# Optimization experiments

Hardware: AMD Instinct MI355X
Metric: run time of the kernel (lower is better)

## Reference

```python
import jax, jax.numpy as jnp
import numpy as np

D_IN = 1024
D_OUT = 1024
NUM_HEADS = 16
HEAD_DIM = D_OUT // NUM_HEADS


def setup_inputs() -> dict:
    key = jax.random.key(0)
    ks = jax.random.split(key, 6)
    s = 0.02
    x = jax.random.normal(ks[0], (1, 4096, D_IN), dtype=jnp.float32)
    W_q = jax.random.normal(ks[1], (D_IN, D_OUT), dtype=jnp.float32) * s
    W_k = jax.random.normal(ks[2], (D_IN, D_OUT), dtype=jnp.float32) * s
    W_v = jax.random.normal(ks[3], (D_IN, D_OUT), dtype=jnp.float32) * s
    W_o = jax.random.normal(ks[4], (D_OUT, D_OUT), dtype=jnp.float32) * s
    b_o = jnp.zeros((D_OUT,), dtype=jnp.float32)
    return {"x": x, "W_q": W_q, "W_k": W_k, "W_v": W_v, "W_o": W_o, "b_o": b_o}


def reference(x, W_q, W_k, W_v, W_o, b_o):
    b, n, _ = x.shape
    # project and split heads: [b, h, n, d]
    def split_heads(t):
        return t.reshape(b, n, NUM_HEADS, HEAD_DIM).transpose(0, 2, 1, 3)
    q = split_heads(x @ W_q)
    k = split_heads(x @ W_k)
    v = split_heads(x @ W_v)
    scale = 1.0 / jnp.sqrt(jnp.float32(HEAD_DIM))
    scores = jnp.einsum('bhqd,bhkd->bhqk', q, k) * scale  # [b,h,n,n]
    causal = jnp.tril(jnp.ones((n, n), dtype=bool))
    scores = jnp.where(causal, scores, -jnp.inf)
    weights = jax.nn.softmax(scores, axis=-1)
    # dropout rate is 0.0 -> identity
    ctx = jnp.einsum('bhqk,bhkd->bhqd', weights, v)
    ctx = ctx.transpose(0, 2, 1, 3).reshape(b, n, D_OUT)
    return ctx @ W_o + b_o
```

## Files before the change

### kernel.cpp

```cpp
#include <hip/hip_runtime.h>
#include <hip/hip_bf16.h>

typedef __hip_bfloat16 bf16;
typedef __attribute__((ext_vector_type(8))) short short8;
typedef __attribute__((ext_vector_type(4))) float floatx4;

#define SEQ 4096
#define DIM 1024
#define NH 16
#define HD 64

#if defined(__has_builtin)
#if __has_builtin(__builtin_amdgcn_exp2f)
#define EXP2(x) __builtin_amdgcn_exp2f(x)
#endif
#endif
#ifndef EXP2
#define EXP2(x) exp2f(x)
#endif

__device__ __forceinline__ short f2s(float f) { bf16 t = __float2bfloat16(f); return *(short*)&t; }

__device__ __forceinline__ void gload16(const void* g, void* l) {
    __builtin_amdgcn_global_load_lds(
        (const __attribute__((address_space(1))) void*)g,
        (__attribute__((address_space(3))) void*)l, 16, 0, 0);
}

__device__ __forceinline__ void barrier_lgkm() {
    asm volatile("s_waitcnt lgkmcnt(0)" ::: "memory");
    __builtin_amdgcn_s_barrier();
}

__device__ __forceinline__ short8 cvt8(float4 a, float4 b) {
    short8 s;
    s[0] = f2s(a.x); s[1] = f2s(a.y); s[2] = f2s(a.z); s[3] = f2s(a.w);
    s[4] = f2s(b.x); s[5] = f2s(b.y); s[6] = f2s(b.z); s[7] = f2s(b.w);
    return s;
}

__global__ __launch_bounds__(256) void transpose_cast_kernel(
    const float* __restrict__ W0, const float* __restrict__ W1,
    const float* __restrict__ W2, const float* __restrict__ W3,
    bf16* __restrict__ Wt_all)
{
    const float* W = blockIdx.z == 0 ? W0 : blockIdx.z == 1 ? W1
                   : blockIdx.z == 2 ? W2 : W3;
    bf16* Wt = Wt_all + (size_t)blockIdx.z * DIM * DIM;

    __shared__ float tile[32][33];
    const int n0 = blockIdx.x * 32, k0 = blockIdx.y * 32;
    const int tr = threadIdx.x >> 5;
    const int tc = threadIdx.x & 31;
#pragma unroll
    for (int i = 0; i < 32; i += 8)
        tile[tr + i][tc] = W[(size_t)(k0 + tr + i) * DIM + n0 + tc];
    __syncthreads();
#pragma unroll
    for (int i = 0; i < 32; i += 8)
        Wt[(size_t)(n0 + tr + i) * DIM + k0 + tc] = __float2bfloat16(tile[tc][tr + i]);
}

#define QBM 128
#define QBN 128
#define QBK 64

__global__ __launch_bounds__(256) void qkv_gemm_kernel(
    const float* __restrict__ A, const bf16* __restrict__ Wt,
    bf16* __restrict__ Qb, bf16* __restrict__ Kb, bf16* __restrict__ Vb)
{
    const int z = blockIdx.z;
    const bf16* Bt = Wt + (size_t)z * DIM * DIM;
    bf16* C = z == 0 ? Qb : (z == 1 ? Kb : Vb);
    const float osc = (z == 0) ? 0.18033688f : 1.0f;

    __shared__ alignas(16) float Af[QBM][QBK];
    __shared__ alignas(16) short Bs[QBN][QBK];

    const int tid  = threadIdx.x;
    const int wave = tid >> 6, lane = tid & 63;
    const int l15  = lane & 15, quad = lane >> 4;
    const int wm = (wave & 1) * 64;
    const int wn = (wave >> 1) * 64;
    const int bm = blockIdx.y * QBM;
    const int bn = blockIdx.x * QBN;

    const int arow = tid >> 4;
    const int agch = (tid & 15) ^ (arow & 15);
    const float* gA = A + (size_t)(bm + arow) * DIM + agch * 4;
    char* ldsA = (char*)&Af[0][0] + wave * 1024;

    const int brow = tid >> 3;
    const int bgch = (tid & 7) ^ (brow & 7);
    const bf16* gB = Bt + (size_t)(bn + brow) * DIM + bgch * 8;
    char* ldsB = (char*)&Bs[0][0] + wave * 1024;

    floatx4 acc[4][4] = {};

    for (int k0 = 0; k0 < DIM; k0 += QBK) {
        __syncthreads();
#pragma unroll
        for (int c = 0; c < 8; ++c)
            gload16(gA + (size_t)c * 16 * DIM + k0, ldsA + c * 4096);
#pragma unroll
        for (int c = 0; c < 4; ++c)
            gload16(gB + (size_t)c * 32 * DIM + k0, ldsB + c * 4096);
        __syncthreads();

#pragma unroll
        for (int c2 = 0; c2 < 2; ++c2) {
            const int g0 = c2 * 8 + quad * 2;
            const int cb = (c2 * 4 + quad) ^ (l15 & 7);
            short8 afr[4], bfr[4];
#pragma unroll
            for (int i = 0; i < 4; ++i) {
                const int ra = wm + i * 16 + l15;
                float4 f0 = *(const float4*)&Af[ra][(g0 ^ l15) * 4];
                float4 f1 = *(const float4*)&Af[ra][((g0 + 1) ^ l15) * 4];
                afr[i] = cvt8(f0, f1);
                bfr[i] = *(const short8*)&Bs[wn + i * 16 + l15][cb * 8];
            }
#pragma unroll
            for (int mi = 0; mi < 4; ++mi)
#pragma unroll
                for (int ni = 0; ni < 4; ++ni)
                    acc[mi][ni] = __builtin_amdgcn_mfma_f32_16x16x32_bf16(
                        afr[mi], bfr[ni], acc[mi][ni], 0, 0, 0);
        }
    }

#pragma unroll
    for (int mi = 0; mi < 4; ++mi)
#pragma unroll
        for (int r = 0; r < 4; ++r) {
            const int row = bm + wm + mi * 16 + quad * 4 + r;
#pragma unroll
            for (int ni = 0; ni < 4; ++ni) {
                const int col = bn + wn + ni * 16 + l15;
                C[(size_t)row * DIM + col] = __float2bfloat16(acc[mi][ni][r] * osc);
            }
        }
}

__global__ __launch_bounds__(256) void out_gemm_kernel(
    const bf16* __restrict__ A, const bf16* __restrict__ Bt,
    const float* __restrict__ bias, float* __restrict__ C)
{
    __shared__ alignas(16) short Asl[128][64];
    __shared__ alignas(16) short Bsl[64][64];

    const int tid  = threadIdx.x;
    const int wave = tid >> 6, lane = tid & 63;
    const int l15  = lane & 15, quad = lane >> 4;
    const int wm = (wave & 1) * 64;
    const int wn = (wave >> 1) * 32;
    const int bm = blockIdx.y * 128;
    const int bn = blockIdx.x * 64;

    const int srow   = tid >> 3;
    const int gchunk = (tid & 7) ^ (srow & 7);
    const bf16* gA = A  + (size_t)(bm + srow) * DIM + gchunk * 8;
    const bf16* gB = Bt + (size_t)(bn + srow) * DIM + gchunk * 8;
    char* ldsA = (char*)&Asl[0][0] + wave * 1024;
    char* ldsB = (char*)&Bsl[0][0] + wave * 1024;

    floatx4 acc[4][2] = {};

    for (int k0 = 0; k0 < DIM; k0 += 64) {
        __syncthreads();
#pragma unroll
        for (int c = 0; c < 4; ++c)
            gload16(gA + (size_t)c * 32 * DIM + k0, ldsA + c * 4096);
#pragma unroll
        for (int c = 0; c < 2; ++c)
            gload16(gB + (size_t)c * 32 * DIM + k0, ldsB + c * 4096);
        __syncthreads();

#pragma unroll
        for (int c2 = 0; c2 < 2; ++c2) {
            const int cb = (c2 * 4 + quad) ^ (l15 & 7);
            short8 afr[4], bfr[2];
#pragma unroll
            for (int i = 0; i < 4; ++i)
                afr[i] = *(const short8*)&Asl[wm + i * 16 + l15][cb * 8];
#pragma unroll
            for (int i = 0; i < 2; ++i)
                bfr[i] = *(const short8*)&Bsl[wn + i * 16 + l15][cb * 8];
#pragma unroll
            for (int mi = 0; mi < 4; ++mi)
#pragma unroll
                for (int ni = 0; ni < 2; ++ni)
                    acc[mi][ni] = __builtin_amdgcn_mfma_f32_16x16x32_bf16(
                        afr[mi], bfr[ni], acc[mi][ni], 0, 0, 0);
        }
    }

#pragma unroll
    for (int mi = 0; mi < 4; ++mi)
#pragma unroll
        for (int r = 0; r < 4; ++r) {
            const int row = bm + wm + mi * 16 + quad * 4 + r;
#pragma unroll
            for (int ni = 0; ni < 2; ++ni) {
                const int col = bn + wn + ni * 16 + l15;
                C[(size_t)row * DIM + col] = acc[mi][ni][r] + bias[col];
            }
        }
}

#define QT 128
#define KT 64
#define LDT 72

__global__ __launch_bounds__(512, 4) void flash_attn_kernel(
    const bf16* __restrict__ Q, const bf16* __restrict__ K,
    const bf16* __restrict__ V, bf16* ctx)
{
    const int lin  = blockIdx.y * 32 + blockIdx.x;
    const int half = lin >> 8, idx = lin & 255;
    const int qj   = half ? (idx & 31) : 31 - (idx & 31);
    const int h    = (idx >> 5) + 8 * half;
    const int q0   = qj * QT;
    const int nkt  = 2 * qj + 2;

    const int tid  = threadIdx.x;
    const int wave = tid >> 6;
    const int qg   = wave & 3;
    const int kh   = wave >> 2;
    const int lane = tid & 63;
    const int l15  = lane & 15;
    const int quad = lane >> 4;

    __shared__ alignas(16) char smem[36864];
    short (*Ks)[KT][LDT] = (short (*)[KT][LDT])smem;
    short (*Vt)[HD][LDT] = (short (*)[HD][LDT])(smem + 18432);
    float* redO = (float*)smem;
    float* redL = (float*)(smem + 32768);

    short8 qfrag[2][2];
#pragma unroll
    for (int s = 0; s < 2; ++s) {
        const bf16* qp = Q + (size_t)(q0 + qg * 32 + s * 16 + l15) * DIM
                       + h * HD + quad * 8;
        qfrag[s][0] = *(const short8*)(qp);
        qfrag[s][1] = *(const short8*)(qp + 32);
    }

    const int kr = tid >> 3, kc = (tid & 7) * 8;
    const bool vstager = tid < 256;
    const int vr = (tid & 31) * 2, vd = ((tid >> 5) & 7) * 8;
    const int vcol = (vr & 32) + ((vr >> 2) & 3) * 8
                   + ((vr >> 4) & 1) * 4 + (vr & 3);

    short8 kreg, vreg0, vreg1;
    kreg = *(const short8*)(K + (size_t)kr * DIM + h * HD + kc);
    if (vstager) {
        vreg0 = *(const short8*)(V + (size_t)vr * DIM + h * HD + vd);
        vreg1 = *(const short8*)(V + (size_t)(vr + 1) * DIM + h * HD + vd);
    }
    *(short8*)&Ks[0][kr][kc] = kreg;
    if (vstager) {
#pragma unroll
        for (int i = 0; i < 8; ++i) {
            unsigned int pv = (unsigned int)(unsigned short)vreg0[i]
                            | ((unsigned int)(unsigned short)vreg1[i] << 16);
            *(unsigned int*)&Vt[0][vd + i][vcol] = pv;
        }
    }
    kreg = *(const short8*)(K + (size_t)(KT + kr) * DIM + h * HD + kc);
    if (vstager) {
        vreg0 = *(const short8*)(V + (size_t)(KT + vr) * DIM + h * HD + vd);
        vreg1 = *(const short8*)(V + (size_t)(KT + vr + 1) * DIM + h * HD + vd);
    }

    barrier_lgkm();

    short8 onesf;
#pragma unroll
    for (int i = 0; i < 8; ++i) onesf[i] = (short)0x3F80;

    floatx4 o_acc[2][4] = {};
    floatx4 lacc[2] = {};

    for (int kt = 0; kt < nkt; ++kt) {
        const int b = kt & 1;

        floatx4 sT[2][2] = {};
#pragma unroll
        for (int n = 0; n < 2; ++n)
#pragma unroll
            for (int c = 0; c < 2; ++c) {
                short8 kf = *(const short8*)
                    &Ks[b][kh * 32 + n * 16 + l15][c * 32 + quad * 8];
#pragma unroll
                for (int s = 0; s < 2; ++s)
                    sT[s][n] = __builtin_amdgcn_mfma_f32_16x16x32_bf16(
                        kf, qfrag[s][c], sT[s][n], 0, 0, 0);
            }

        if (kt + 1 < nkt) {
            *(short8*)&Ks[b ^ 1][kr][kc] = kreg;
            if (vstager) {
#pragma unroll
                for (int i = 0; i < 8; ++i) {
                    unsigned int pv = (unsigned int)(unsigned short)vreg0[i]
                                    | ((unsigned int)(unsigned short)vreg1[i] << 16);
                    *(unsigned int*)&Vt[b ^ 1][vd + i][vcol] = pv;
                }
            }
            if (kt + 2 < nkt) {
                const size_t nb = (size_t)(kt + 2) * KT;
                kreg = *(const short8*)(K + (nb + kr) * DIM + h * HD + kc);
                if (vstager) {
                    vreg0 = *(const short8*)(V + (nb + vr) * DIM + h * HD + vd);
                    vreg1 = *(const short8*)(V + (nb + vr + 1) * DIM + h * HD + vd);
                }
            }
        }

        short8 pfrag[2];
        const int kbase = kt * KT + kh * 32;
        if (kt >= nkt - 2) {
#pragma unroll
            for (int s = 0; s < 2; ++s) {
                const int qrow = q0 + qg * 32 + s * 16 + l15;
                float p[2][4];
#pragma unroll
                for (int n = 0; n < 2; ++n) {
                    const int key0 = kbase + n * 16 + quad * 4;
#pragma unroll
                    for (int r = 0; r < 4; ++r)
                        p[n][r] = (key0 + r <= qrow) ? EXP2(sT[s][n][r]) : 0.f;
                }
                short8 f;
#pragma unroll
                for (int j = 0; j < 8; ++j)
                    f[j] = f2s(p[j >> 2][j & 3]);
                pfrag[s] = f;
            }
        } else {
#pragma unroll
            for (int s = 0; s < 2; ++s) {
                short8 f;
#pragma unroll
                for (int j = 0; j < 8; ++j)
                    f[j] = f2s(EXP2(sT[s][j >> 2][j & 3]));
                pfrag[s] = f;
            }
        }

#pragma unroll
        for (int n = 0; n < 4; ++n) {
            short8 vf = *(const short8*)
                &Vt[b][n * 16 + l15][kh * 32 + quad * 8];
#pragma unroll
            for (int s = 0; s < 2; ++s)
                o_acc[s][n] = __builtin_amdgcn_mfma_f32_16x16x32_bf16(
                    pfrag[s], vf, o_acc[s][n], 0, 0, 0);
        }
#pragma unroll
        for (int s = 0; s < 2; ++s)
            lacc[s] = __builtin_amdgcn_mfma_f32_16x16x32_bf16(
                pfrag[s], onesf, lacc[s], 0, 0, 0);

        barrier_lgkm();
    }

    if (kh == 1) {
#pragma unroll
        for (int s = 0; s < 2; ++s)
#pragma unroll
            for (int n = 0; n < 4; ++n)
#pragma unroll
                for (int r = 0; r < 4; ++r)
                    redO[(size_t)(qg * 32 + s * 16 + quad * 4 + r) * 64
                         + n * 16 + l15] = o_acc[s][n][r];
        if (l15 == 0) {
#pragma unroll
            for (int s = 0; s < 2; ++s)
#pragma unroll
                for (int r = 0; r < 4; ++r)
                    redL[qg * 32 + s * 16 + quad * 4 + r] = lacc[s][r];
        }
    }
    __syncthreads();
    if (kh == 0) {
#pragma unroll
        for (int s = 0; s < 2; ++s)
#pragma unroll
            for (int r = 0; r < 4; ++r) {
                const int row_l = qg * 32 + s * 16 + quad * 4 + r;
                const float lsum = lacc[s][r] + redL[row_l];
                const float inv = 1.0f / lsum;
                const int row = q0 + row_l;
#pragma unroll
                for (int n = 0; n < 4; ++n) {
                    const float o = o_acc[s][n][r]
                                  + redO[(size_t)row_l * 64 + n * 16 + l15];
                    ctx[(size_t)row * DIM + h * HD + n * 16 + l15] =
                        __float2bfloat16(o * inv);
                }
            }
    }
}

extern "C" void kernel_launch(void* const* d_in, const int* in_sizes, int n_in,
                              void* d_out, int out_size, void* d_ws, size_t ws_size,
                              hipStream_t stream)
{
    const float* x  = (const float*)d_in[0];
    const float* Wq = (const float*)d_in[1];
    const float* Wk = (const float*)d_in[2];
    const float* Wv = (const float*)d_in[3];
    const float* Wo = (const float*)d_in[4];
    const float* bo = (const float*)d_in[5];
    float* out = (float*)d_out;

    bf16* Wt_all = (bf16*)d_ws;
    bf16* Qb     = Wt_all + (size_t)4 * DIM * DIM;
    bf16* V      = (bf16*)d_out;
    bf16* Kb     = V + (size_t)SEQ * DIM;
    bf16* ctx    = Qb;
    const bf16* Wot = Wt_all + (size_t)3 * DIM * DIM;

    transpose_cast_kernel<<<dim3(32, 32, 4), 256, 0, stream>>>(Wq, Wk, Wv, Wo, Wt_all);

    qkv_gemm_kernel<<<dim3(DIM / QBN, SEQ / QBM, 3), 256, 0, stream>>>(
        x, Wt_all, Qb, Kb, V);

    flash_attn_kernel<<<dim3(32, NH), 512, 0, stream>>>(Qb, Kb, V, ctx);

    out_gemm_kernel<<<dim3(DIM / 64, SEQ / 128), 256, 0, stream>>>(
        ctx, Wot, bo, out);
}
```

Baseline: 184.3 us.

## Software-pipeline flash attention: overlap QK^T of next tile with PV of previous

Restructures the attention loop into a two-stage software pipeline: each iteration computes S for tile p while finishing exp/PV for tile p-1, using a triple-buffered LDS ring for K and V^T. The aim is to hide the exp/convert latency behind independent MFMA work and to keep the matrix units busy. In exchange it raises LDS use from 36KB to 54KB per block, which may lower occupancy under launch_bounds(512,4), and adds live registers for the carried score tile.

```diff
diff --git a/kernel.cpp b/kernel.cpp
--- a/kernel.cpp
+++ b/kernel.cpp
@@ -211,6 +211,7 @@
 #define QT 128
 #define KT 64
 #define LDT 72
+#define BUFB 18432
 
 __global__ __launch_bounds__(512, 4) void flash_attn_kernel(
     const bf16* __restrict__ Q, const bf16* __restrict__ K,
@@ -231,9 +232,9 @@
     const int l15  = lane & 15;
     const int quad = lane >> 4;
 
-    __shared__ alignas(16) char smem[36864];
-    short (*Ks)[KT][LDT] = (short (*)[KT][LDT])smem;
-    short (*Vt)[HD][LDT] = (short (*)[HD][LDT])(smem + 18432);
+    __shared__ alignas(16) char smem[3 * BUFB];
+#define KSB(b) ((short(*)[LDT])(smem + (size_t)(b) * BUFB))
+#define VTB(b) ((short(*)[LDT])(smem + (size_t)(b) * BUFB + 9216))
     float* redO = (float*)smem;
     float* redL = (float*)(smem + 32768);
 
@@ -258,13 +259,13 @@
         vreg0 = *(const short8*)(V + (size_t)vr * DIM + h * HD + vd);
         vreg1 = *(const short8*)(V + (size_t)(vr + 1) * DIM + h * HD + vd);
     }
-    *(short8*)&Ks[0][kr][kc] = kreg;
+    *(short8*)&KSB(0)[kr][kc] = kreg;
     if (vstager) {
 #pragma unroll
         for (int i = 0; i < 8; ++i) {
             unsigned int pv = (unsigned int)(unsigned short)vreg0[i]
                             | ((unsigned int)(unsigned short)vreg1[i] << 16);
-            *(unsigned int*)&Vt[0][vd + i][vcol] = pv;
+            *(unsigned int*)&VTB(0)[vd + i][vcol] = pv;
         }
     }
     kreg = *(const short8*)(K + (size_t)(KT + kr) * DIM + h * HD + kc);
@@ -281,35 +282,93 @@
 
     floatx4 o_acc[2][4] = {};
     floatx4 lacc[2] = {};
-
-    for (int kt = 0; kt < nkt; ++kt) {
-        const int b = kt & 1;
-
-        floatx4 sT[2][2] = {};
+    floatx4 sTp[2][2] = {};
+
+#define FINISH(t) do {                                                        \
+    short(*_Vtb)[LDT] = VTB((t) % 3);                                         \
+    short8 _vf[4];                                                            \
+    _Pragma("unroll")                                                         \
+    for (int _n = 0; _n < 4; ++_n)                                            \
+        _vf[_n] = *(const short8*)&_Vtb[_n * 16 + l15][kh * 32 + quad * 8];   \
+    short8 _pf[2];                                                            \
+    const int _kbase = (t) * KT + kh * 32;                                    \
+    if ((t) >= nkt - 2) {                                                     \
+        _Pragma("unroll")                                                     \
+        for (int _s = 0; _s < 2; ++_s) {                                      \
+            const int _qrow = q0 + qg * 32 + _s * 16 + l15;                   \
+            float _p[2][4];                                                   \
+            _Pragma("unroll")                                                 \
+            for (int _n = 0; _n < 2; ++_n) {                                  \
+                const int _k0 = _kbase + _n * 16 + quad * 4;                  \
+                _Pragma("unroll")                                             \
+                for (int _r = 0; _r < 4; ++_r)                                \
+                    _p[_n][_r] = (_k0 + _r <= _qrow)                          \
+                               ? EXP2(sTp[_s][_n][_r]) : 0.f;                 \
+            }                                                                 \
+            short8 _f;                                                        \
+            _Pragma("unroll")                                                 \
+            for (int _j = 0; _j < 8; ++_j)                                    \
+                _f[_j] = f2s(_p[_j >> 2][_j & 3]);                            \
+            _pf[_s] = _f;                                                     \
+        }                                                                     \
+    } else {                                                                  \
+        _Pragma("unroll")                                                     \
+        for (int _s = 0; _s < 2; ++_s) {                                      \
+            short8 _f;                                                        \
+            _Pragma("unroll")                                                 \
+            for (int _j = 0; _j < 8; ++_j)                                    \
+                _f[_j] = f2s(EXP2(sTp[_s][_j >> 2][_j & 3]));                 \
+            _pf[_s] = _f;                                                     \
+        }                                                                     \
+    }                                                                         \
+    _Pragma("unroll")                                                         \
+    for (int _n = 0; _n < 4; ++_n)                                            \
+        _Pragma("unroll")                                                     \
+        for (int _s = 0; _s < 2; ++_s)                                        \
+            o_acc[_s][_n] = __builtin_amdgcn_mfma_f32_16x16x32_bf16(          \
+                _pf[_s], _vf[_n], o_acc[_s][_n], 0, 0, 0);                    \
+    _Pragma("unroll")                                                         \
+    for (int _s = 0; _s < 2; ++_s)                                            \
+        lacc[_s] = __builtin_amdgcn_mfma_f32_16x16x32_bf16(                   \
+            _pf[_s], onesf, lacc[_s], 0, 0, 0);                               \
+} while (0)
+
+    for (int p = 0; p < nkt; ++p) {
+        short(*Ksb)[LDT] = KSB(p % 3);
+
+        short8 kf[2][2];
 #pragma unroll
         for (int n = 0; n < 2; ++n)
 #pragma unroll
-            for (int c = 0; c < 2; ++c) {
-                short8 kf = *(const short8*)
-                    &Ks[b][kh * 32 + n * 16 + l15][c * 32 + quad * 8];
-#pragma unroll
-                for (int s = 0; s < 2; ++s)
-                    sT[s][n] = __builtin_amdgcn_mfma_f32_16x16x32_bf16(
-                        kf, qfrag[s][c], sT[s][n], 0, 0, 0);
-            }
-
-        if (kt + 1 < nkt) {
-            *(short8*)&Ks[b ^ 1][kr][kc] = kreg;
+            for (int c = 0; c < 2; ++c)
+                kf[n][c] = *(const short8*)
+                    &Ksb[kh * 32 + n * 16 + l15][c * 32 + quad * 8];
+
+        if (p > 0) FINISH(p - 1);
+
+#pragma unroll
+        for (int s = 0; s < 2; ++s)
+#pragma unroll
+            for (int n = 0; n < 2; ++n) {
+                floatx4 t = {};
+                t = __builtin_amdgcn_mfma_f32_16x16x32_bf16(
+                    kf[n][0], qfrag[s][0], t, 0, 0, 0);
+                sTp[s][n] = __builtin_amdgcn_mfma_f32_16x16x32_bf16(
+                    kf[n][1], qfrag[s][1], t, 0, 0, 0);
+            }
+
+        if (p + 1 < nkt) {
+            *(short8*)&KSB((p + 1) % 3)[kr][kc] = kreg;
             if (vstager) {
 #pragma unroll
                 for (int i = 0; i < 8; ++i) {
                     unsigned int pv = (unsigned int)(unsigned short)vreg0[i]
                                     | ((unsigned int)(unsigned short)vreg1[i] << 16);
-                    *(unsigned int*)&Vt[b ^ 1][vd + i][vcol] = pv;
+                    *(unsigned int*)&VTB((p + 1) % 3)[vd + i][vcol] = pv;
                 }
             }
-            if (kt + 2 < nkt) {
-                const size_t nb = (size_t)(kt + 2) * KT;
+            if (p + 2 < nkt) {
+                const size_t nb = (size_t)(p + 2) * KT;
                 kreg = *(const short8*)(K + (nb + kr) * DIM + h * HD + kc);
                 if (vstager) {
                     vreg0 = *(const short8*)(V + (nb + vr) * DIM + h * HD + vd);
@@ -318,53 +377,12 @@
             }
         }
 
-        short8 pfrag[2];
-        const int kbase = kt * KT + kh * 32;
-        if (kt >= nkt - 2) {
-#pragma unroll
-            for (int s = 0; s < 2; ++s) {
-                const int qrow = q0 + qg * 32 + s * 16 + l15;
-                float p[2][4];
-#pragma unroll
-                for (int n = 0; n < 2; ++n) {
-                    const int key0 = kbase + n * 16 + quad * 4;
-#pragma unroll
-                    for (int r = 0; r < 4; ++r)
-                        p[n][r] = (key0 + r <= qrow) ? EXP2(sT[s][n][r]) : 0.f;
-                }
-                short8 f;
-#pragma unroll
-                for (int j = 0; j < 8; ++j)
-                    f[j] = f2s(p[j >> 2][j & 3]);
-                pfrag[s] = f;
-            }
-        } else {
-#pragma unroll
-            for (int s = 0; s < 2; ++s) {
-                short8 f;
-#pragma unroll
-                for (int j = 0; j < 8; ++j)
-                    f[j] = f2s(EXP2(sT[s][j >> 2][j & 3]));
-                pfrag[s] = f;
-            }
-        }
-
-#pragma unroll
-        for (int n = 0; n < 4; ++n) {
-            short8 vf = *(const short8*)
-                &Vt[b][n * 16 + l15][kh * 32 + quad * 8];
-#pragma unroll
-            for (int s = 0; s < 2; ++s)
-                o_acc[s][n] = __builtin_amdgcn_mfma_f32_16x16x32_bf16(
-                    pfrag[s], vf, o_acc[s][n], 0, 0, 0);
-        }
-#pragma unroll
-        for (int s = 0; s < 2; ++s)
-            lacc[s] = __builtin_amdgcn_mfma_f32_16x16x32_bf16(
-                pfrag[s], onesf, lacc[s], 0, 0, 0);
-
         barrier_lgkm();
     }
+
+    FINISH(nkt - 1);
+    barrier_lgkm();
+#undef FINISH
 
     if (kh == 1) {
 #pragma unroll
@@ -402,6 +420,8 @@
                 }
             }
     }
+#undef KSB
+#undef VTB
 }
 
 extern "C" void kernel_launch(void* const* d_in, const int* in_sizes, int n_in,
```

Measured after the change: 187.7 us. Within noise of the previous version (+1.8%).

## Split long causal query tiles across two blocks and merge with a combine kernel

Applied to the files above, without the earlier changes.

The causal attention grid becomes 768 blocks. Query strips 16–31 are split into two halves along the key range, each computed by its own block. The first half writes an unnormalized partial output and row sums to workspace, the second half writes into ctx. A new combine kernel then sums the two parts and normalizes. This targets load imbalance, where the longest query tiles walk twice as many key tiles as the average and set the critical path. The cost is an extra kernel launch, extra global traffic for the partials, and bf16 rounding of the partial outputs before they are combined.

```diff
diff --git a/kernel.cpp b/kernel.cpp
--- a/kernel.cpp
+++ b/kernel.cpp
@@ -20,6 +20,7 @@
 #endif
 
 __device__ __forceinline__ short f2s(float f) { bf16 t = __float2bfloat16(f); return *(short*)&t; }
+__device__ __forceinline__ float s2f(short s) { bf16 t = *(bf16*)&s; return __bfloat162float(t); }
 
 __device__ __forceinline__ void gload16(const void* g, void* l) {
     __builtin_amdgcn_global_load_lds(
@@ -214,14 +215,22 @@
 
 __global__ __launch_bounds__(512, 4) void flash_attn_kernel(
     const bf16* __restrict__ Q, const bf16* __restrict__ K,
-    const bf16* __restrict__ V, bf16* ctx)
-{
-    const int lin  = blockIdx.y * 32 + blockIdx.x;
-    const int half = lin >> 8, idx = lin & 255;
-    const int qj   = half ? (idx & 31) : 31 - (idx & 31);
-    const int h    = (idx >> 5) + 8 * half;
-    const int q0   = qj * QT;
-    const int nkt  = 2 * qj + 2;
+    const bf16* __restrict__ V, bf16* ctx,
+    bf16* __restrict__ O0buf, float* __restrict__ l0buf,
+    float* __restrict__ l1buf)
+{
+    const int blk = blockIdx.x;
+    const int g   = blk >> 8;
+    const int i   = blk & 255;
+    const int t   = i & 15, h = i >> 4;
+
+    int qj, kt0, kt1;
+    if (g == 2) { qj = t;      kt0 = 0;      kt1 = 2 * t + 2; }
+    else        { qj = 31 - t; kt0 = g ? (qj + 1) : 0;
+                               kt1 = g ? (2 * qj + 2) : (qj + 1); }
+    const int nkt = 2 * qj + 2;
+    const int q0  = qj * QT;
+    const int sp  = (15 - t) * 16 + h;
 
     const int tid  = threadIdx.x;
     const int wave = tid >> 6;
@@ -253,37 +262,43 @@
                    + ((vr >> 4) & 1) * 4 + (vr & 3);
 
     short8 kreg, vreg0, vreg1;
-    kreg = *(const short8*)(K + (size_t)kr * DIM + h * HD + kc);
-    if (vstager) {
-        vreg0 = *(const short8*)(V + (size_t)vr * DIM + h * HD + vd);
-        vreg1 = *(const short8*)(V + (size_t)(vr + 1) * DIM + h * HD + vd);
+    {
+        const size_t kb = (size_t)kt0 * KT;
+        kreg = *(const short8*)(K + (kb + kr) * DIM + h * HD + kc);
+        if (vstager) {
+            vreg0 = *(const short8*)(V + (kb + vr) * DIM + h * HD + vd);
+            vreg1 = *(const short8*)(V + (kb + vr + 1) * DIM + h * HD + vd);
+        }
     }
     *(short8*)&Ks[0][kr][kc] = kreg;
     if (vstager) {
 #pragma unroll
-        for (int i = 0; i < 8; ++i) {
-            unsigned int pv = (unsigned int)(unsigned short)vreg0[i]
-                            | ((unsigned int)(unsigned short)vreg1[i] << 16);
-            *(unsigned int*)&Vt[0][vd + i][vcol] = pv;
-        }
-    }
-    kreg = *(const short8*)(K + (size_t)(KT + kr) * DIM + h * HD + kc);
-    if (vstager) {
-        vreg0 = *(const short8*)(V + (size_t)(KT + vr) * DIM + h * HD + vd);
-        vreg1 = *(const short8*)(V + (size_t)(KT + vr + 1) * DIM + h * HD + vd);
+        for (int i2 = 0; i2 < 8; ++i2) {
+            unsigned int pv = (unsigned int)(unsigned short)vreg0[i2]
+                            | ((unsigned int)(unsigned short)vreg1[i2] << 16);
+            *(unsigned int*)&Vt[0][vd + i2][vcol] = pv;
+        }
+    }
+    {
+        const size_t kb = (size_t)(kt0 + 1) * KT;
+        kreg = *(const short8*)(K + (kb + kr) * DIM + h * HD + kc);
+        if (vstager) {
+            vreg0 = *(const short8*)(V + (kb + vr) * DIM + h * HD + vd);
+            vreg1 = *(const short8*)(V + (kb + vr + 1) * DIM + h * HD + vd);
+        }
     }
 
     barrier_lgkm();
 
     short8 onesf;
 #pragma unroll
-    for (int i = 0; i < 8; ++i) onesf[i] = (short)0x3F80;
+    for (int i2 = 0; i2 < 8; ++i2) onesf[i2] = (short)0x3F80;
 
     floatx4 o_acc[2][4] = {};
     floatx4 lacc[2] = {};
 
-    for (int kt = 0; kt < nkt; ++kt) {
-        const int b = kt & 1;
+    for (int kt = kt0; kt < kt1; ++kt) {
+        const int b = (kt - kt0) & 1;
 
         floatx4 sT[2][2] = {};
 #pragma unroll
@@ -298,17 +313,17 @@
                         kf, qfrag[s][c], sT[s][n], 0, 0, 0);
             }
 
-        if (kt + 1 < nkt) {
+        if (kt + 1 < kt1) {
             *(short8*)&Ks[b ^ 1][kr][kc] = kreg;
             if (vstager) {
 #pragma unroll
-                for (int i = 0; i < 8; ++i) {
-                    unsigned int pv = (unsigned int)(unsigned short)vreg0[i]
-                                    | ((unsigned int)(unsigned short)vreg1[i] << 16);
-                    *(unsigned int*)&Vt[b ^ 1][vd + i][vcol] = pv;
+                for (int i2 = 0; i2 < 8; ++i2) {
+                    unsigned int pv = (unsigned int)(unsigned short)vreg0[i2]
+                                    | ((unsigned int)(unsigned short)vreg1[i2] << 16);
+                    *(unsigned int*)&Vt[b ^ 1][vd + i2][vcol] = pv;
                 }
             }
-            if (kt + 2 < nkt) {
+            if (kt + 2 < kt1) {
                 const size_t nb = (size_t)(kt + 2) * KT;
                 kreg = *(const short8*)(K + (nb + kr) * DIM + h * HD + kc);
                 if (vstager) {
@@ -391,17 +406,59 @@
             for (int r = 0; r < 4; ++r) {
                 const int row_l = qg * 32 + s * 16 + quad * 4 + r;
                 const float lsum = lacc[s][r] + redL[row_l];
-                const float inv = 1.0f / lsum;
-                const int row = q0 + row_l;
-#pragma unroll
-                for (int n = 0; n < 4; ++n) {
-                    const float o = o_acc[s][n][r]
-                                  + redO[(size_t)row_l * 64 + n * 16 + l15];
-                    ctx[(size_t)row * DIM + h * HD + n * 16 + l15] =
-                        __float2bfloat16(o * inv);
+                if (g == 2) {
+                    const float inv = 1.0f / lsum;
+                    const int row = q0 + row_l;
+#pragma unroll
+                    for (int n = 0; n < 4; ++n) {
+                        const float o = o_acc[s][n][r]
+                                      + redO[(size_t)row_l * 64 + n * 16 + l15];
+                        ctx[(size_t)row * DIM + h * HD + n * 16 + l15] =
+                            __float2bfloat16(o * inv);
+                    }
+                } else if (g == 0) {
+#pragma unroll
+                    for (int n = 0; n < 4; ++n) {
+                        const float o = o_acc[s][n][r]
+                                      + redO[(size_t)row_l * 64 + n * 16 + l15];
+                        O0buf[(size_t)sp * 8192 + row_l * 64 + n * 16 + l15] =
+                            __float2bfloat16(o);
+                    }
+                    if (l15 == 0) l0buf[sp * 128 + row_l] = lsum;
+                } else {
+                    const int row = q0 + row_l;
+#pragma unroll
+                    for (int n = 0; n < 4; ++n) {
+                        const float o = o_acc[s][n][r]
+                                      + redO[(size_t)row_l * 64 + n * 16 + l15];
+                        ctx[(size_t)row * DIM + h * HD + n * 16 + l15] =
+                            __float2bfloat16(o);
+                    }
+                    if (l15 == 0) l1buf[sp * 128 + row_l] = lsum;
                 }
             }
     }
+}
+
+__global__ __launch_bounds__(512) void combine_kernel(
+    const bf16* __restrict__ O0buf, const float* __restrict__ l0buf,
+    const float* __restrict__ l1buf, bf16* __restrict__ ctx)
+{
+    const int tid = blockIdx.x * 512 + threadIdx.x;
+    const int d8  = tid & 7;
+    const int row = (tid >> 3) & 127;
+    const int sp  = tid >> 10;
+    const int strip = 16 + (sp >> 4), h = sp & 15;
+
+    const float inv = 1.0f / (l0buf[sp * 128 + row] + l1buf[sp * 128 + row]);
+    const short8 a = *(const short8*)&O0buf[(size_t)sp * 8192 + row * 64 + d8 * 8];
+    bf16* cp = ctx + (size_t)(strip * 128 + row) * DIM + h * HD + d8 * 8;
+    short8 c = *(const short8*)cp;
+    short8 o;
+#pragma unroll
+    for (int j = 0; j < 8; ++j)
+        o[j] = f2s((s2f(a[j]) + s2f(c[j])) * inv);
+    *(short8*)cp = o;
 }
 
 extern "C" void kernel_launch(void* const* d_in, const int* in_sizes, int n_in,
@@ -423,12 +480,19 @@
     bf16* ctx    = Qb;
     const bf16* Wot = Wt_all + (size_t)3 * DIM * DIM;
 
+    bf16*  O0buf = (bf16*)d_ws;
+    float* l0buf = (float*)((char*)d_ws + (4u << 20));
+    float* l1buf = (float*)((char*)d_ws + (4u << 20) + (128u << 10));
+
     transpose_cast_kernel<<<dim3(32, 32, 4), 256, 0, stream>>>(Wq, Wk, Wv, Wo, Wt_all);
 
     qkv_gemm_kernel<<<dim3(DIM / QBN, SEQ / QBM, 3), 256, 0, stream>>>(
         x, Wt_all, Qb, Kb, V);
 
-    flash_attn_kernel<<<dim3(32, NH), 512, 0, stream>>>(Qb, Kb, V, ctx);
+    flash_attn_kernel<<<dim3(768), 512, 0, stream>>>(
+        Qb, Kb, V, ctx, O0buf, l0buf, l1buf);
+
+    combine_kernel<<<dim3(512), 512, 0, stream>>>(O0buf, l0buf, l1buf, ctx);
 
     out_gemm_kernel<<<dim3(DIM / 64, SEQ / 128), 256, 0, stream>>>(
         ctx, Wot, bo, out);
```

After: 194.9 us. +5.8%, slower.
